# Kernel tuning notes

Hardware: AMD Instinct MI355X
Metric: run time of the kernel (lower is better)

The kernel has to match this reference:

```python
import jax, jax.numpy as jnp
import numpy as np

N_E = 1024     # codebook size (n_e, nbooks=1)
E_DIM = 256    # embedding dim
BETA = 0.25
B, T = 16, 4096


def setup_inputs() -> dict:
    key = jax.random.key(0)
    k1, k2 = jax.random.split(key)
    z = jax.random.normal(k1, (B, T, E_DIM), dtype=jnp.float32)
    # matches torch init: uniform(-1/n_e_i, 1/n_e_i)
    codebook = jax.random.uniform(k2, (N_E, E_DIM), dtype=jnp.float32,
                                  minval=-1.0 / N_E, maxval=1.0 / N_E)
    return {"z": z, "codebook": codebook}


def reference(z, codebook):
    zf = z.reshape(-1, E_DIM)                                   # [N, d]
    dist = (jnp.sum(zf * zf, axis=1, keepdims=True)
            - 2.0 * (zf @ codebook.T)
            + jnp.sum(codebook * codebook, axis=1)[None, :])
    idx = jnp.argmin(dist, axis=1)                              # [N]
    # one-hot scatter + matmul == codebook gather
    z_q = codebook[idx].reshape(z.shape)                        # [B, T, d]
    loss = (jnp.mean((z_q - jax.lax.stop_gradient(z)) ** 2)
            + BETA * jnp.mean((z - jax.lax.stop_gradient(z_q)) ** 2))
    # straight-through estimator
    z_q_st = z + jax.lax.stop_gradient(z_q - z)
    indices = idx.reshape(z.shape[:-1] + (1,))                  # [B, T, 1]
    return z_q_st, loss, indices
```

## Files before the change

kernel.cpp:

```cpp
#include <hip/hip_runtime.h>
#include <hip/hip_bf16.h>
#include <math.h>

typedef __bf16 bf16x8 __attribute__((ext_vector_type(8)));
typedef float f32x4 __attribute__((ext_vector_type(4)));
typedef unsigned short u16x8 __attribute__((ext_vector_type(8)));

constexpr int EDIM = 256;
constexpr int NE = 1024;
constexpr int NROWS = 65536;
constexpr float BETA = 0.25f;

constexpr size_t A2T_OFF   = 0;
constexpr size_t A2T_SZ    = (size_t)512 * 16 * 8192;
constexpr size_t B2T_OFF   = A2T_OFF + A2T_SZ;
constexpr size_t B2T_SZ    = (size_t)8 * 16 * 8192;
constexpr size_t SZROW_OFF = B2T_OFF + B2T_SZ;
constexpr size_t SZABS_OFF = SZROW_OFF + 262144;
constexpr size_t CNORM_OFF = SZABS_OFF + 262144;
constexpr size_t BMAX_OFF  = CNORM_OFF + 4096;
constexpr size_t EMAX_OFF  = BMAX_OFF + 4096;
constexpr size_t CNT_OFF   = EMAX_OFF + 256;
constexpr size_t LIST_OFF  = CNT_OFF + 256;
constexpr size_t LPART_OFF = LIST_OFF + 262144;
constexpr size_t LP2_OFF   = LPART_OFF + 262144;
constexpr size_t WS_NEED   = LP2_OFF + 1024;

__device__ __forceinline__ unsigned short f32_to_bf16_rne(float f) {
    unsigned u = __float_as_uint(f);
    u += 0x7fffu + ((u >> 16) & 1u);
    return (unsigned short)(u >> 16);
}
__device__ __forceinline__ float bf16_to_f32(unsigned short h) {
    return __uint_as_float((unsigned)h << 16);
}

#define GLL16(g, l)                                                                   \
    __builtin_amdgcn_global_load_lds(                                                 \
        (const __attribute__((address_space(1))) unsigned int*)(g),                   \
        (__attribute__((address_space(3))) unsigned int*)(l), 16, 0, 0)

__global__ __launch_bounds__(256)
void p1_rowstats(const float* __restrict__ z, float* __restrict__ szrow,
                 float* __restrict__ szabs) {
    __shared__ float xr[4][256];
    __shared__ float rres[4][16];
    const int w = threadIdx.x >> 6, l = threadIdx.x & 63;
    const int row = blockIdx.x * 4 + w;
    const float4 v = reinterpret_cast<const float4*>(z + (size_t)row * EDIM)[l];
    *reinterpret_cast<float4*>(&xr[w][l * 4]) = v;
    float asum = fabsf(v.x) + fabsf(v.y) + fabsf(v.z) + fabsf(v.w);
    #pragma unroll
    for (int off = 32; off; off >>= 1) asum += __shfl_down(asum, off);
    __syncthreads();
    if (l < 16) {
        const float* x = xr[w] + (l >> 3) * 128;
        const int j = l & 7;
        float r = __fmul_rn(x[j], x[j]);
        for (int i = 8; i < 128; i += 8) r = __fadd_rn(r, __fmul_rn(x[i + j], x[i + j]));
        rres[w][l] = r;
    }
    __syncthreads();
    if (l == 0) {
        const float* rr = rres[w];
        float h0 = __fadd_rn(__fadd_rn(__fadd_rn(rr[0], rr[1]), __fadd_rn(rr[2], rr[3])),
                             __fadd_rn(__fadd_rn(rr[4], rr[5]), __fadd_rn(rr[6], rr[7])));
        float h1 = __fadd_rn(__fadd_rn(__fadd_rn(rr[8], rr[9]), __fadd_rn(rr[10], rr[11])),
                             __fadd_rn(__fadd_rn(rr[12], rr[13]), __fadd_rn(rr[14], rr[15])));
        szrow[row] = __fadd_rn(h0, h1);
        szabs[row] = asum;
    }
}

__global__ __launch_bounds__(64)
void p3_codebook(const float* __restrict__ cb, float* __restrict__ cnorm,
                 char* __restrict__ B2t, float* __restrict__ bmax) {
    __shared__ float xr[256];
    __shared__ float rres[16];
    __shared__ unsigned short ehi[256], elo[256];
    const int e = blockIdx.x, l = threadIdx.x;
    const float4 v = reinterpret_cast<const float4*>(cb + (size_t)e * EDIM)[l];
    *reinterpret_cast<float4*>(&xr[l * 4]) = v;
    float amax = fmaxf(fmaxf(fabsf(v.x), fabsf(v.y)), fmaxf(fabsf(v.z), fabsf(v.w)));
    #pragma unroll
    for (int off = 32; off; off >>= 1) amax = fmaxf(amax, __shfl_down(amax, off));
    __syncthreads();
    #pragma unroll
    for (int i = 0; i < 4; ++i) {
        const int idx = i * 64 + l;
        const float f = xr[idx];
        const unsigned short h = f32_to_bf16_rne(f);
        ehi[idx] = h;
        elo[idx] = f32_to_bf16_rne(f - bf16_to_f32(h));
    }
    if (l < 16) {
        const float* x = xr + (l >> 3) * 128;
        const int j = l & 7;
        float r = __fmul_rn(x[j], x[j]);
        for (int i = 8; i < 128; i += 8) r = __fadd_rn(r, __fmul_rn(x[i + j], x[i + j]));
        rres[l] = r;
    }
    __syncthreads();
    if (l == 0) {
        float h0 = __fadd_rn(__fadd_rn(__fadd_rn(rres[0], rres[1]), __fadd_rn(rres[2], rres[3])),
                             __fadd_rn(__fadd_rn(rres[4], rres[5]), __fadd_rn(rres[6], rres[7])));
        float h1 = __fadd_rn(__fadd_rn(__fadd_rn(rres[8], rres[9]), __fadd_rn(rres[10], rres[11])),
                             __fadd_rn(__fadd_rn(rres[12], rres[13]), __fadd_rn(rres[14], rres[15])));
        cnorm[e] = __fadd_rn(h0, h1);
        bmax[e] = amax;
    }
    {
        const int c = l >> 2, kgv = l & 3;
        const int colbase = ((c < 8) ? c * 32 : (c - 8) * 32) + kgv * 8;
        const unsigned short* src = (c < 8) ? ehi : elo;
        char* dst = B2t + ((((size_t)(e >> 7) * 16 + c) * 512 + (size_t)kgv * 128 + (e & 127)) * 16);
        *reinterpret_cast<uint4*>(dst) = *reinterpret_cast<const uint4*>(&src[colbase]);
    }
}

__global__ void k_emax(const float* __restrict__ bmax, float* __restrict__ emax, int* cnt) {
    __shared__ float red[256];
    if (threadIdx.x == 0) cnt[0] = 0;
    float m = 0.f;
    for (int i = threadIdx.x; i < NE; i += 256) m = fmaxf(m, bmax[i]);
    red[threadIdx.x] = m;
    __syncthreads();
    for (int h = 128; h; h >>= 1) {
        if (threadIdx.x < h) red[threadIdx.x] = fmaxf(red[threadIdx.x], red[threadIdx.x + h]);
        __syncthreads();
    }
    if (threadIdx.x == 0) emax[0] = red[0];
}

__global__ __launch_bounds__(256)
void p2_atile(const float* __restrict__ z, char* __restrict__ A2t) {
    __shared__ float t[128][66];
    const int mt = blockIdx.x, cq = blockIdx.y, tid = threadIdx.x;
    const int c0 = cq * 64;
    #pragma unroll
    for (int i = 0; i < 8; ++i) {
        const int fid = i * 256 + tid;
        const int r = fid >> 4, c4 = fid & 15;
        const float4 v = *reinterpret_cast<const float4*>(
            z + ((size_t)(mt * 128 + r)) * EDIM + c0 + c4 * 4);
        *reinterpret_cast<float4*>(&t[r][c4 * 4]) = v;
    }
    __syncthreads();
    #pragma unroll
    for (int i = 0; i < 8; ++i) {
        const int sid = i * 256 + tid;
        const int caq = sid >> 9, kgv = (sid >> 7) & 3, rw = sid & 127;
        const int coff = (caq & 1) * 32 + kgv * 8;
        const int ca = (caq < 2) ? (cq * 2 + caq) : (8 + cq * 2 + (caq - 2));
        u16x8 out;
        #pragma unroll
        for (int j = 0; j < 8; ++j) {
            const float f = t[rw][coff + j];
            unsigned short h = f32_to_bf16_rne(f);
            if (caq >= 2) h = f32_to_bf16_rne(f - bf16_to_f32(h));
            out[j] = h;
        }
        char* dst = A2t + ((((size_t)mt * 16 + ca) * 512 + (size_t)kgv * 128 + rw) * 16);
        *reinterpret_cast<u16x8*>(dst) = out;
    }
}

__global__ __launch_bounds__(256, 1)
void vq_main(const char* __restrict__ A2t, const char* __restrict__ B2t,
             const float* __restrict__ cnorm, const float* __restrict__ szrow,
             const float* __restrict__ szabs, const float* __restrict__ emaxp,
             const float* __restrict__ cb,
             float* __restrict__ idxf, int* __restrict__ cnt, int* __restrict__ list,
             float* __restrict__ zq, float* __restrict__ lpart) {
    constexpr int RING = 131072;
    constexpr int CNS  = 155648;
    __shared__ char smem[159744] __attribute__((aligned(16)));
    float* cns = reinterpret_cast<float*>(smem + CNS);
    float (*ms1)[2] = reinterpret_cast<float(*)[2]>(smem);
    float (*ms2)[2] = reinterpret_cast<float(*)[2]>(smem + 1024);
    int   (*mi1)[2] = reinterpret_cast<int(*)[2]>(smem + 2048);
    int*  bidx      = reinterpret_cast<int*>(smem + 3072);

    const int tid = threadIdx.x;
    const int mtile = blockIdx.x;
    const size_t rowbase = (size_t)mtile * 128;
    const int l = tid & 63, wid = tid >> 6;
    const int kg = l >> 4, li = l & 15;
    const int wr = wid >> 1, wc = wid & 1;

    GLL16((const char*)cnorm + tid * 16, smem + CNS + tid * 16);
    const char* Ag = A2t + (size_t)mtile * 131072;
    #pragma unroll
    for (int i = 0; i < 32; ++i)
        GLL16(Ag + (i * 256 + tid) * 16, smem + (i * 256 + tid) * 16);
    #pragma unroll
    for (int c = 0; c < 2; ++c) {
        const char* gb = B2t + (size_t)c * 8192;
        char* lb = smem + RING + c * 8192;
        GLL16(gb + tid * 16, lb + tid * 16);
        GLL16(gb + (tid + 256) * 16, lb + (tid + 256) * 16);
    }

    int aoff[4], boff[4];
    #pragma unroll
    for (int f = 0; f < 4; ++f) {
        aoff[f] = kg * 2048 + (wr * 64 + f * 16 + li) * 16;
        boff[f] = kg * 2048 + (wc * 64 + f * 16 + li) * 16;
    }

    float s1v[4][4], s2v[4][4];
    int i1v[4][4];
    #pragma unroll
    for (int a = 0; a < 4; ++a)
        #pragma unroll
        for (int b = 0; b < 4; ++b) { s1v[a][b] = 3.4e38f; s2v[a][b] = 3.4e38f; i1v[a][b] = 0; }

    for (int nt = 0; nt < 8; ++nt) {
        const int ntm3 = nt % 3;
        f32x4 acc[4][4];
        const f32x4 zf4 = {0.f, 0.f, 0.f, 0.f};
        #pragma unroll
        for (int a = 0; a < 4; ++a)
            #pragma unroll
            for (int b = 0; b < 4; ++b) acc[a][b] = zf4;

        #pragma unroll
        for (int j = 0; j < 16; ++j) {
            asm volatile("s_waitcnt vmcnt(2)" ::: "memory");
            __builtin_amdgcn_s_barrier();
            {
                int gs = nt * 16 + j + 2;
                if (gs >= 128) gs -= 128;
                int ss = ntm3 + ((j + 2) % 3);
                if (ss >= 3) ss -= 3;
                const char* gb = B2t + (size_t)gs * 8192;
                char* lb = smem + RING + ss * 8192;
                GLL16(gb + tid * 16, lb + tid * 16);
                GLL16(gb + (tid + 256) * 16, lb + (tid + 256) * 16);
            }
            int sc = ntm3 + (j % 3);
            if (sc >= 3) sc -= 3;
            const char* Bb = smem + RING + sc * 8192;
            bf16x8 bfr[4];
            #pragma unroll
            for (int fn = 0; fn < 4; ++fn)
                bfr[fn] = *reinterpret_cast<const bf16x8*>(Bb + boff[fn]);
            if (j < 8) {
                bf16x8 afH[4], afL[4];
                #pragma unroll
                for (int fm = 0; fm < 4; ++fm) {
                    afH[fm] = *reinterpret_cast<const bf16x8*>(smem + j * 8192 + aoff[fm]);
                    afL[fm] = *reinterpret_cast<const bf16x8*>(smem + (8 + j) * 8192 + aoff[fm]);
                }
                #pragma unroll
                for (int fm = 0; fm < 4; ++fm)
                    #pragma unroll
                    for (int fn = 0; fn < 4; ++fn)
                        acc[fm][fn] = __builtin_amdgcn_mfma_f32_16x16x32_bf16(afH[fm], bfr[fn], acc[fm][fn], 0, 0, 0);
                #pragma unroll
                for (int fm = 0; fm < 4; ++fm)
                    #pragma unroll
                    for (int fn = 0; fn < 4; ++fn)
                        acc[fm][fn] = __builtin_amdgcn_mfma_f32_16x16x32_bf16(afL[fm], bfr[fn], acc[fm][fn], 0, 0, 0);
            } else {
                bf16x8 af[4];
                #pragma unroll
                for (int fm = 0; fm < 4; ++fm)
                    af[fm] = *reinterpret_cast<const bf16x8*>(smem + (j - 8) * 8192 + aoff[fm]);
                #pragma unroll
                for (int fm = 0; fm < 4; ++fm)
                    #pragma unroll
                    for (int fn = 0; fn < 4; ++fn)
                        acc[fm][fn] = __builtin_amdgcn_mfma_f32_16x16x32_bf16(af[fm], bfr[fn], acc[fm][fn], 0, 0, 0);
            }
        }

        const int ntb = nt * 128;
        #pragma unroll
        for (int fn = 0; fn < 4; ++fn) {
            const int e = ntb + wc * 64 + fn * 16 + li;
            const float cn = cns[e];
            #pragma unroll
            for (int fm = 0; fm < 4; ++fm)
                #pragma unroll
                for (int r = 0; r < 4; ++r) {
                    const float s = cn - 2.0f * acc[fm][fn][r];
                    if (s < s1v[fm][r]) { s2v[fm][r] = s1v[fm][r]; s1v[fm][r] = s; i1v[fm][r] = e; }
                    else s2v[fm][r] = fminf(s2v[fm][r], s);
                }
        }
    }

    __syncthreads();

    #pragma unroll
    for (int fm = 0; fm < 4; ++fm)
        #pragma unroll
        for (int r = 0; r < 4; ++r) {
            float s1 = s1v[fm][r], s2 = s2v[fm][r];
            int i1 = i1v[fm][r];
            #pragma unroll
            for (int off = 1; off < 16; off <<= 1) {
                const float os1 = __shfl_xor(s1, off);
                const float os2 = __shfl_xor(s2, off);
                const int oi1 = __shfl_xor(i1, off);
                const bool take = (os1 < s1) || (os1 == s1 && oi1 < i1);
                const float loser = take ? s1 : os1;
                if (take) { s1 = os1; i1 = oi1; }
                s2 = fminf(fminf(s2, os2), loser);
            }
            if (li == 0) {
                const int rloc = wr * 64 + fm * 16 + (kg << 2) + r;
                ms1[rloc][wc] = s1; ms2[rloc][wc] = s2; mi1[rloc][wc] = i1;
            }
        }
    __syncthreads();

    if (tid < 128) {
        const float a1 = ms1[tid][0], b1 = ms1[tid][1];
        const float a2 = ms2[tid][0], b2 = ms2[tid][1];
        const int ai = mi1[tid][0], bi = mi1[tid][1];
        const bool take = (b1 < a1) || (b1 == a1 && bi < ai);
        const float s1 = take ? b1 : a1;
        const int i1 = take ? bi : ai;
        const float loser = take ? a1 : b1;
        const float s2 = fminf(fminf(a2, b2), loser);
        const int rowg = (int)rowbase + tid;
        const float szv = szrow[rowg], sab = szabs[rowg];
        const float M = 2.0e-4f * sab * emaxp[0] + ldexpf(1.0f, ilogbf(szv * 1.02f) - 23);
        idxf[rowg] = (float)i1;
        lpart[rowg] = s1 + szv;
        bidx[tid] = i1;
        if (s2 - s1 <= 2.0f * M) { const int p = atomicAdd(cnt, 1); list[p] = rowg; }
    }
    __syncthreads();

    {
        const float4* cb4 = reinterpret_cast<const float4*>(cb);
        float4* zq4 = reinterpret_cast<float4*>(zq);
        #pragma unroll 4
        for (int j = 0; j < 32; ++j) {
            const int rr = wid * 32 + j;
            const int e = bidx[rr];
            zq4[(rowbase + rr) * 64 + l] = cb4[(size_t)e * 64 + l];
        }
    }
}

__global__ __launch_bounds__(256)
void vq_rescan(const float* __restrict__ z, const float* __restrict__ cb,
               const float* __restrict__ cnorm, const float* __restrict__ szrow,
               const int* __restrict__ list, const int* __restrict__ cntp,
               float* __restrict__ idxf, float* __restrict__ zq, float* __restrict__ lpart) {
    __shared__ float zr[8][260];
    __shared__ float szs[8];
    __shared__ int rows_s[8];
    __shared__ float sred[256];
    __shared__ int ired[256];
    const int tid = threadIdx.x;
    const int n = cntp[0];
    const int groups = (n + 7) >> 3;
    for (int g = blockIdx.x; g < groups; g += gridDim.x) {
        if (tid < 8) {
            const int gi = g * 8 + tid;
            const int row = (gi < n) ? list[gi] : -1;
            rows_s[tid] = row;
            szs[tid] = (row >= 0) ? szrow[row] : 0.f;
        }
        __syncthreads();
        #pragma unroll
        for (int i = 0; i < 8; ++i) {
            const int sid = i * 256 + tid;
            const int rr = sid >> 8, k = sid & 255;
            if (rows_s[rr] >= 0) zr[rr][k] = z[(size_t)rows_s[rr] * EDIM + k];
        }
        __syncthreads();
        float bs[8];
        int bi[8];
        #pragma unroll
        for (int rr = 0; rr < 8; ++rr) { bs[rr] = 3.4e38f; bi[rr] = 0; }
        for (int q = 0; q < 4; ++q) {
            const int e = tid + q * 256;
            const float4* crow = reinterpret_cast<const float4*>(cb + (size_t)e * EDIM);
            float d[8];
            #pragma unroll
            for (int rr = 0; rr < 8; ++rr) d[rr] = 0.f;
            for (int k4 = 0; k4 < 64; ++k4) {
                const float4 c4 = crow[k4];
                #pragma unroll
                for (int rr = 0; rr < 8; ++rr) {
                    d[rr] = fmaf(zr[rr][k4 * 4 + 0], c4.x, d[rr]);
                    d[rr] = fmaf(zr[rr][k4 * 4 + 1], c4.y, d[rr]);
                    d[rr] = fmaf(zr[rr][k4 * 4 + 2], c4.z, d[rr]);
                    d[rr] = fmaf(zr[rr][k4 * 4 + 3], c4.w, d[rr]);
                }
            }
            const float cn = cnorm[e];
            #pragma unroll
            for (int rr = 0; rr < 8; ++rr) {
                const float b1 = __fadd_rn(szs[rr], __fmul_rn(-2.0f, d[rr]));
                const float s = __fadd_rn(b1, cn);
                if (s < bs[rr]) { bs[rr] = s; bi[rr] = e; }
            }
        }
        #pragma unroll
        for (int rr = 0; rr < 8; ++rr) {
            sred[tid] = bs[rr];
            ired[tid] = bi[rr];
            __syncthreads();
            for (int h = 128; h; h >>= 1) {
                if (tid < h) {
                    const float so = sred[tid + h];
                    const int io = ired[tid + h];
                    if (so < sred[tid] || (so == sred[tid] && io < ired[tid])) {
                        sred[tid] = so; ired[tid] = io;
                    }
                }
                __syncthreads();
            }
            if (rows_s[rr] >= 0) {
                const int best = ired[0];
                const int row = rows_s[rr];
                zq[(size_t)row * EDIM + tid] = cb[(size_t)best * EDIM + tid];
                if (tid == 0) { idxf[row] = (float)best; lpart[row] = sred[0]; }
            }
            __syncthreads();
        }
    }
}

__global__ void vq_loss1(const float* __restrict__ lpart, float* __restrict__ lp2) {
    __shared__ float red[256];
    const int t = threadIdx.x;
    red[t] = lpart[blockIdx.x * 256 + t];
    __syncthreads();
    for (int h = 128; h; h >>= 1) {
        if (t < h) red[t] += red[t + h];
        __syncthreads();
    }
    if (t == 0) lp2[blockIdx.x] = red[0];
}
__global__ void vq_loss2(const float* __restrict__ lp2, float* __restrict__ outloss) {
    __shared__ float red[256];
    const int t = threadIdx.x;
    red[t] = lp2[t];
    __syncthreads();
    for (int h = 128; h; h >>= 1) {
        if (t < h) red[t] += red[t + h];
        __syncthreads();
    }
    if (t == 0) outloss[0] = red[0] * ((1.0f + BETA) / 16777216.0f);
}

__device__ __forceinline__ float np_sum128_sq(const float* __restrict__ x) {
    float r[8];
    #pragma unroll
    for (int j = 0; j < 8; ++j) r[j] = __fmul_rn(x[j], x[j]);
    #pragma unroll
    for (int i = 8; i < 128; i += 8)
        #pragma unroll
        for (int j = 0; j < 8; ++j) r[j] = __fadd_rn(r[j], __fmul_rn(x[i + j], x[i + j]));
    return __fadd_rn(__fadd_rn(__fadd_rn(r[0], r[1]), __fadd_rn(r[2], r[3])),
                     __fadd_rn(__fadd_rn(r[4], r[5]), __fadd_rn(r[6], r[7])));
}
__global__ void fb_prep(const float* __restrict__ z, const float* __restrict__ cb,
                        float* __restrict__ szrow, float* __restrict__ cnorm) {
    int t = blockIdx.x * blockDim.x + threadIdx.x;
    if (t < NROWS) {
        const float* x = z + (size_t)t * EDIM;
        szrow[t] = __fadd_rn(np_sum128_sq(x), np_sum128_sq(x + 128));
    } else if (t < NROWS + NE) {
        const float* x = cb + (size_t)(t - NROWS) * EDIM;
        cnorm[t - NROWS] = __fadd_rn(np_sum128_sq(x), np_sum128_sq(x + 128));
    }
}
__global__ __launch_bounds__(256, 2)
void fb_vq(const float* __restrict__ z, const float* __restrict__ cb,
           const float* __restrict__ cnorm, const float* __restrict__ szrow,
           float* __restrict__ zq, float* __restrict__ idxf, float* __restrict__ lpart) {
    __shared__ float As[64 * 268];
    __shared__ float Bs[32 * 68];
    __shared__ int bidx[64];
    __shared__ float lred[4];
    const int tid = threadIdx.x;
    const int tx = tid & 15, ty = tid >> 4;
    const size_t rowbase = (size_t)blockIdx.x * 64;
    const float4* zg = reinterpret_cast<const float4*>(z + rowbase * EDIM);
    #pragma unroll
    for (int it = 0; it < 16; ++it) {
        int id = it * 256 + tid;
        int r = id >> 6, c4 = id & 63;
        float4 v = zg[id];
        *reinterpret_cast<float4*>(&As[r * 268 + c4 * 4]) = v;
    }
    float sz[4];
    #pragma unroll
    for (int m = 0; m < 4; ++m) sz[m] = szrow[rowbase + ty * 4 + m];
    float bestS[4]; int bestI[4];
    #pragma unroll
    for (int m = 0; m < 4; ++m) { bestS[m] = 3.4e38f; bestI[m] = 0; }
    for (int nt = 0; nt < NE / 64; ++nt) {
        float acc[4][4];
        #pragma unroll
        for (int m = 0; m < 4; ++m)
            #pragma unroll
            for (int n = 0; n < 4; ++n) acc[m][n] = 0.f;
        const int ebase = nt * 64;
        for (int k0 = 0; k0 < EDIM; k0 += 32) {
            __syncthreads();
            #pragma unroll
            for (int i = 0; i < 8; ++i) {
                int id = i * 256 + tid;
                int n = id >> 5, k = id & 31;
                Bs[k * 68 + n] = cb[(size_t)(ebase + n) * EDIM + k0 + k];
            }
            __syncthreads();
            #pragma unroll
            for (int kg2 = 0; kg2 < 32; kg2 += 4) {
                float4 a[4], b[4];
                #pragma unroll
                for (int m = 0; m < 4; ++m)
                    a[m] = *reinterpret_cast<const float4*>(&As[(ty * 4 + m) * 268 + k0 + kg2]);
                #pragma unroll
                for (int kk = 0; kk < 4; ++kk)
                    b[kk] = *reinterpret_cast<const float4*>(&Bs[(kg2 + kk) * 68 + tx * 4]);
                #pragma unroll
                for (int m = 0; m < 4; ++m) {
                    const float* av = reinterpret_cast<const float*>(&a[m]);
                    #pragma unroll
                    for (int kk = 0; kk < 4; ++kk) {
                        acc[m][0] = fmaf(av[kk], b[kk].x, acc[m][0]);
                        acc[m][1] = fmaf(av[kk], b[kk].y, acc[m][1]);
                        acc[m][2] = fmaf(av[kk], b[kk].z, acc[m][2]);
                        acc[m][3] = fmaf(av[kk], b[kk].w, acc[m][3]);
                    }
                }
            }
        }
        #pragma unroll
        for (int n = 0; n < 4; ++n) {
            int e = ebase + tx * 4 + n;
            float cn = cnorm[e];
            #pragma unroll
            for (int m = 0; m < 4; ++m) {
                float b1 = __fadd_rn(sz[m], __fmul_rn(-2.0f, acc[m][n]));
                float s = __fadd_rn(b1, cn);
                if (s < bestS[m]) { bestS[m] = s; bestI[m] = e; }
            }
        }
    }
    #pragma unroll
    for (int m = 0; m < 4; ++m) {
        float s = bestS[m]; int i = bestI[m];
        #pragma unroll
        for (int off = 1; off < 16; off <<= 1) {
            float s2 = __shfl_xor(s, off);
            int i2 = __shfl_xor(i, off);
            if (s2 < s || (s2 == s && i2 < i)) { s = s2; i = i2; }
        }
        if (tx == 0) bidx[ty * 4 + m] = i;
    }
    __syncthreads();
    if (tid < 64) idxf[rowbase + tid] = (float)bidx[tid];
    float lsum = 0.f;
    for (int r = 0; r < 64; ++r) {
        int e = bidx[r];
        float c = cb[(size_t)e * EDIM + tid];
        float zv = As[r * 268 + tid];
        float d = c - zv;
        lsum = fmaf(d, d, lsum);
        zq[(rowbase + r) * EDIM + tid] = c;
    }
    #pragma unroll
    for (int off = 32; off; off >>= 1) lsum += __shfl_down(lsum, off);
    if ((tid & 63) == 0) lred[tid >> 6] = lsum;
    __syncthreads();
    if (tid == 0) lpart[blockIdx.x] = lred[0] + lred[1] + lred[2] + lred[3];
}
__global__ void fb_loss(const float* __restrict__ lpart, float* __restrict__ out_loss) {
    __shared__ float red[256];
    int tid = threadIdx.x;
    float s = 0.f;
    for (int i = tid; i < NROWS / 64; i += 256) s += lpart[i];
    red[tid] = s;
    __syncthreads();
    for (int h = 128; h; h >>= 1) {
        if (tid < h) red[tid] += red[tid + h];
        __syncthreads();
    }
    if (tid == 0) out_loss[0] = red[0] * (1.0f + BETA) / (float)((size_t)NROWS * EDIM);
}

extern "C" void kernel_launch(void* const* d_in, const int* in_sizes, int n_in,
                              void* d_out, int out_size, void* d_ws, size_t ws_size,
                              hipStream_t stream) {
    const float* z = (const float*)d_in[0];
    const float* cb = (const float*)d_in[1];
    float* out = (float*)d_out;
    float* zq = out;
    float* loss = out + (size_t)NROWS * EDIM;
    float* idxf = loss + 1;
    char* ws = (char*)d_ws;

    if (ws_size < WS_NEED) {
        float* cnorm = (float*)ws;
        float* szrow = cnorm + NE;
        float* lpart = szrow + NROWS;
        hipLaunchKernelGGL(fb_prep, dim3((NROWS + NE + 255) / 256), dim3(256), 0, stream, z, cb, szrow, cnorm);
        hipLaunchKernelGGL(fb_vq, dim3(NROWS / 64), dim3(256), 0, stream, z, cb, cnorm, szrow, zq, idxf, lpart);
        hipLaunchKernelGGL(fb_loss, dim3(1), dim3(256), 0, stream, lpart, loss);
        return;
    }

    char* A2t = ws + A2T_OFF;
    char* B2t = ws + B2T_OFF;
    float* szrow = (float*)(ws + SZROW_OFF);
    float* szabs = (float*)(ws + SZABS_OFF);
    float* cnorm = (float*)(ws + CNORM_OFF);
    float* bmax = (float*)(ws + BMAX_OFF);
    float* emax = (float*)(ws + EMAX_OFF);
    int* cnt = (int*)(ws + CNT_OFF);
    int* list = (int*)(ws + LIST_OFF);
    float* lpart = (float*)(ws + LPART_OFF);
    float* lp2 = (float*)(ws + LP2_OFF);

    hipLaunchKernelGGL(p1_rowstats, dim3(NROWS / 4), dim3(256), 0, stream, z, szrow, szabs);
    hipLaunchKernelGGL(p3_codebook, dim3(NE), dim3(64), 0, stream, cb, cnorm, B2t, bmax);
    hipLaunchKernelGGL(k_emax, dim3(1), dim3(256), 0, stream, bmax, emax, cnt);
    hipLaunchKernelGGL(p2_atile, dim3(512, 4), dim3(256), 0, stream, z, A2t);
    hipLaunchKernelGGL(vq_main, dim3(512), dim3(256), 0, stream,
                       A2t, B2t, cnorm, szrow, szabs, emax, cb, idxf, cnt, list, zq, lpart);
    hipLaunchKernelGGL(vq_rescan, dim3(1024), dim3(256), 0, stream,
                       z, cb, cnorm, szrow, list, cnt, idxf, zq, lpart);
    hipLaunchKernelGGL(vq_loss1, dim3(256), dim3(256), 0, stream, lpart, lp2);
    hipLaunchKernelGGL(vq_loss2, dim3(1), dim3(256), 0, stream, lp2, loss);
}
```

Baseline: 248.1 us.

## Register double-buffer LDS fragments and deepen codebook ring prefetch

Fragments for the next k-step are now read from LDS into registers while the current step's MFMAs run, so LDS read latency overlaps matrix math. The global-to-LDS prefetch distance grows from 2 to 3 slots in the 3-slot ring. Boundary conditions drop the wraparound loads at the tail. This costs extra VGPRs for the second fragment set and adds an lgkmcnt(0) wait before every barrier.

```diff
diff --git a/kernel.cpp b/kernel.cpp
--- a/kernel.cpp
+++ b/kernel.cpp
@@ -194,12 +194,14 @@
     for (int i = 0; i < 32; ++i)
         GLL16(Ag + (i * 256 + tid) * 16, smem + (i * 256 + tid) * 16);
     #pragma unroll
-    for (int c = 0; c < 2; ++c) {
+    for (int c = 0; c < 3; ++c) {
         const char* gb = B2t + (size_t)c * 8192;
         char* lb = smem + RING + c * 8192;
         GLL16(gb + tid * 16, lb + tid * 16);
         GLL16(gb + (tid + 256) * 16, lb + (tid + 256) * 16);
     }
+    asm volatile("s_waitcnt vmcnt(0)" ::: "memory");
+    __builtin_amdgcn_s_barrier();
 
     int aoff[4], boff[4];
     #pragma unroll
@@ -208,6 +210,14 @@
         boff[f] = kg * 2048 + (wc * 64 + f * 16 + li) * 16;
     }
 
+    bf16x8 cAh[4], cAl[4], cB[4];
+    #pragma unroll
+    for (int f = 0; f < 4; ++f) {
+        cAh[f] = *reinterpret_cast<const bf16x8*>(smem + 0 * 8192 + aoff[f]);
+        cAl[f] = *reinterpret_cast<const bf16x8*>(smem + 8 * 8192 + aoff[f]);
+        cB[f]  = *reinterpret_cast<const bf16x8*>(smem + RING + 0 * 8192 + boff[f]);
+    }
+
     float s1v[4][4], s2v[4][4];
     int i1v[4][4];
     #pragma unroll
@@ -216,7 +226,7 @@
         for (int b = 0; b < 4; ++b) { s1v[a][b] = 3.4e38f; s2v[a][b] = 3.4e38f; i1v[a][b] = 0; }
 
     for (int nt = 0; nt < 8; ++nt) {
-        const int ntm3 = nt % 3;
+        int ntm3 = nt; if (ntm3 >= 6) ntm3 -= 6; else if (ntm3 >= 3) ntm3 -= 3;
         f32x4 acc[4][4];
         const f32x4 zf4 = {0.f, 0.f, 0.f, 0.f};
         #pragma unroll
@@ -226,53 +236,54 @@
 
         #pragma unroll
         for (int j = 0; j < 16; ++j) {
-            asm volatile("s_waitcnt vmcnt(2)" ::: "memory");
+            if (nt == 7 && j >= 14) asm volatile("s_waitcnt vmcnt(0)" ::: "memory");
+            else                    asm volatile("s_waitcnt vmcnt(1)" ::: "memory");
+            asm volatile("s_waitcnt lgkmcnt(0)" ::: "memory");
             __builtin_amdgcn_s_barrier();
-            {
-                int gs = nt * 16 + j + 2;
-                if (gs >= 128) gs -= 128;
-                int ss = ntm3 + ((j + 2) % 3);
+            if (!(nt == 7 && j >= 13)) {
+                const int gs = nt * 16 + j + 3;
+                int ss = ntm3 + (j % 3);
                 if (ss >= 3) ss -= 3;
                 const char* gb = B2t + (size_t)gs * 8192;
                 char* lb = smem + RING + ss * 8192;
                 GLL16(gb + tid * 16, lb + tid * 16);
                 GLL16(gb + (tid + 256) * 16, lb + (tid + 256) * 16);
             }
-            int sc = ntm3 + (j % 3);
-            if (sc >= 3) sc -= 3;
-            const char* Bb = smem + RING + sc * 8192;
-            bf16x8 bfr[4];
-            #pragma unroll
-            for (int fn = 0; fn < 4; ++fn)
-                bfr[fn] = *reinterpret_cast<const bf16x8*>(Bb + boff[fn]);
+            bf16x8 nAh[4], nAl[4], nB[4];
+            if (!(nt == 7 && j == 15)) {
+                const int jn = (j + 1) & 15;
+                int sp = ntm3 + ((j + 1) % 3);
+                if (sp >= 3) sp -= 3;
+                const char* Bb = smem + RING + sp * 8192;
+                #pragma unroll
+                for (int f = 0; f < 4; ++f)
+                    nB[f] = *reinterpret_cast<const bf16x8*>(Bb + boff[f]);
+                if (jn < 8) {
+                    #pragma unroll
+                    for (int f = 0; f < 4; ++f) {
+                        nAh[f] = *reinterpret_cast<const bf16x8*>(smem + jn * 8192 + aoff[f]);
+                        nAl[f] = *reinterpret_cast<const bf16x8*>(smem + (8 + jn) * 8192 + aoff[f]);
+                    }
+                } else {
+                    #pragma unroll
+                    for (int f = 0; f < 4; ++f)
+                        nAh[f] = *reinterpret_cast<const bf16x8*>(smem + (jn - 8) * 8192 + aoff[f]);
+                }
+            }
+            #pragma unroll
+            for (int fm = 0; fm < 4; ++fm)
+                #pragma unroll
+                for (int fn = 0; fn < 4; ++fn)
+                    acc[fm][fn] = __builtin_amdgcn_mfma_f32_16x16x32_bf16(cAh[fm], cB[fn], acc[fm][fn], 0, 0, 0);
             if (j < 8) {
-                bf16x8 afH[4], afL[4];
-                #pragma unroll
-                for (int fm = 0; fm < 4; ++fm) {
-                    afH[fm] = *reinterpret_cast<const bf16x8*>(smem + j * 8192 + aoff[fm]);
-                    afL[fm] = *reinterpret_cast<const bf16x8*>(smem + (8 + j) * 8192 + aoff[fm]);
-                }
                 #pragma unroll
                 for (int fm = 0; fm < 4; ++fm)
                     #pragma unroll
                     for (int fn = 0; fn < 4; ++fn)
-                        acc[fm][fn] = __builtin_amdgcn_mfma_f32_16x16x32_bf16(afH[fm], bfr[fn], acc[fm][fn], 0, 0, 0);
-                #pragma unroll
-                for (int fm = 0; fm < 4; ++fm)
-                    #pragma unroll
-                    for (int fn = 0; fn < 4; ++fn)
-                        acc[fm][fn] = __builtin_amdgcn_mfma_f32_16x16x32_bf16(afL[fm], bfr[fn], acc[fm][fn], 0, 0, 0);
-            } else {
-                bf16x8 af[4];
-                #pragma unroll
-                for (int fm = 0; fm < 4; ++fm)
-                    af[fm] = *reinterpret_cast<const bf16x8*>(smem + (j - 8) * 8192 + aoff[fm]);
-                #pragma unroll
-                for (int fm = 0; fm < 4; ++fm)
-                    #pragma unroll
-                    for (int fn = 0; fn < 4; ++fn)
-                        acc[fm][fn] = __builtin_amdgcn_mfma_f32_16x16x32_bf16(af[fm], bfr[fn], acc[fm][fn], 0, 0, 0);
-            }
+                        acc[fm][fn] = __builtin_amdgcn_mfma_f32_16x16x32_bf16(cAl[fm], cB[fn], acc[fm][fn], 0, 0, 0);
+            }
+            #pragma unroll
+            for (int f = 0; f < 4; ++f) { cAh[f] = nAh[f]; cAl[f] = nAl[f]; cB[f] = nB[f]; }
         }
 
         const int ntb = nt * 128;
```

Measured after the change: 266.9 us. +7.6%, slower.
